# Kernel optimization log

Measured on AMD Instinct MI355X. Metric: run time of the kernel, lower is better.

The kernel has to match this reference:

```python
import math
import jax, jax.numpy as jnp
import numpy as np

HEAD_NUM = 8
DIM = 512
D_K = DIM // HEAD_NUM  # 64
M_FEAT = 256
B, L = 4, 2048
STAB = 1e-5


def _orthogonal_gaussian(m, d, rng):
    num_squares = m // d
    blocks = []
    for _ in range(num_squares):
        q, _ = np.linalg.qr(rng.standard_normal((d, d)))
        blocks.append(q.T)
    rem = m - d * num_squares
    if rem:
        q, _ = np.linalg.qr(rng.standard_normal((d, d)))
        blocks.append(q.T[:rem])
    mat = np.concatenate(blocks, axis=0)
    mat = mat / math.sqrt(num_squares + rem / d)
    return mat.astype(np.float32)


def setup_inputs() -> dict:
    key = jax.random.key(0)
    ks = jax.random.split(key, 12)
    rng = np.random.default_rng(0)
    inp = {
        'query': jax.random.normal(ks[0], (B, L, DIM), jnp.float32),
        'key': jax.random.normal(ks[1], (B, L, DIM), jnp.float32),
        'value': jax.random.normal(ks[2], (B, L, DIM), jnp.float32),
        'proj': jnp.asarray(_orthogonal_gaussian(M_FEAT, D_K, rng)),  # [M, d_k]
        'w_q_w': jax.random.normal(ks[3], (DIM, DIM), jnp.float32) * 0.02,
        'w_q_b': jnp.zeros((DIM,), jnp.float32),
        'w_k_w': jax.random.normal(ks[4], (DIM, DIM), jnp.float32) * 0.02,
        'w_k_b': jnp.zeros((DIM,), jnp.float32),
        'w_v_w': jax.random.normal(ks[5], (DIM, DIM), jnp.float32) * 0.02,
        'w_v_b': jnp.zeros((DIM,), jnp.float32),
        'w_o_w': jax.random.normal(ks[6], (DIM, DIM), jnp.float32) * 0.02,
        'w_o_b': jnp.zeros((DIM,), jnp.float32),
    }
    return inp


def _relu_kernel(data, proj):
    # data: [B,L,H,D], proj: [M,D] -> [B,L,H,M]
    ratio = 1.0 / math.sqrt(proj.shape[0])
    return jax.nn.relu(ratio * jnp.einsum('blhd,md->blhm', data, proj)) + STAB


def _favor_causal(qp, kp, vs):
    # qp, kp: [L,B,H,M]; vs: [L,B,H,D] -> num [L,B,H,D], den [L,B,H]
    b, h, m = qp.shape[1], qp.shape[2], qp.shape[3]
    d = vs.shape[3]
    carry0 = (jnp.zeros((b, h, m, d), qp.dtype), jnp.zeros((b, h, m), qp.dtype))

    def step(carry, inp):
        s_kv, s_k = carry
        q_l, k_l, v_l = inp
        s_kv = s_kv + jnp.einsum('bhm,bhd->bhmd', k_l, v_l)
        s_k = s_k + k_l
        num = jnp.einsum('bhmd,bhm->bhd', s_kv, q_l)
        den = jnp.sum(q_l * s_k, axis=-1)
        return (s_kv, s_k), (num, den)

    _, (num, den) = jax.lax.scan(step, carry0, (qp, kp, vs))
    return num, den


def reference(query, key, value, proj, w_q_w, w_q_b, w_k_w, w_k_b, w_v_w, w_v_b, w_o_w, w_o_b):
    bsz = query.shape[0]
    q = (query @ w_q_w.T + w_q_b).reshape(bsz, -1, HEAD_NUM, D_K)
    k = (key @ w_k_w.T + w_k_b).reshape(bsz, -1, HEAD_NUM, D_K)
    v = (value @ w_v_w.T + w_v_b).reshape(bsz, -1, HEAD_NUM, D_K)
    qp = jnp.swapaxes(_relu_kernel(q, proj), 0, 1)  # [L,B,H,M]
    kp = jnp.swapaxes(_relu_kernel(k, proj), 0, 1)
    vs = jnp.swapaxes(v, 0, 1)                      # [L,B,H,D]
    num, den = _favor_causal(qp, kp, vs)
    attn = jnp.swapaxes(num, 0, 1) / jnp.swapaxes(den, 0, 1)[..., None]  # [B,L,H,D]
    attn = attn.reshape(bsz, -1, HEAD_NUM * D_K)
    return attn @ w_o_w.T + w_o_b
```

## Files before the change

kernel.cpp:

```cpp
#include <hip/hip_runtime.h>
#include <stdint.h>

#define B_ 4
#define L_ 2048
#define H_ 8
#define DK 64
#define M_ 256
#define DIM_ 512
#define NTOK (B_ * L_)
#define CHK 128
#define NC (L_ / CHK)
#define BH (B_ * H_)
#define RATIO 0.0625f
#define STABC 1e-5f

typedef unsigned short ushort_t;
typedef __attribute__((ext_vector_type(8))) short bf8v;
typedef __attribute__((ext_vector_type(4))) float f4v;

#define MFMA16(a, b, c) __builtin_amdgcn_mfma_f32_16x16x32_bf16(a, b, c, 0, 0, 0)

__device__ __forceinline__ ushort_t f2bf(float f) {
  uint32_t u = __float_as_uint(f);
  return (ushort_t)((u + 0x7fffu + ((u >> 16) & 1u)) >> 16);
}
__device__ __forceinline__ float bf2f(ushort_t u) { return __uint_as_float(((uint32_t)u) << 16); }

__device__ __forceinline__ void gll16(const void* g, void* l) {
  __builtin_amdgcn_global_load_lds((const __attribute__((address_space(1))) void*)g,
                                   (__attribute__((address_space(3))) void*)l, 16, 0, 0);
}

__device__ __forceinline__ bf8v ldfrag(const ushort_t* base, int row, int cb) {
  return *(const bf8v*)((const char*)base + row * 128 + (cb ^ ((row & 7) << 4)));
}
__device__ __forceinline__ bf8v ldfrag256(const ushort_t* base, int row, int cb) {
  return *(const bf8v*)((const char*)base + row * 256 + (cb ^ ((row & 7) << 4)));
}
__device__ __forceinline__ bf8v ldfrag512(const ushort_t* base, int row, int cb) {
  return *(const bf8v*)((const char*)base + row * 512 + (cb ^ ((row & 7) << 4)));
}

__global__ __launch_bounds__(256) void cvt_w(const float* __restrict__ wq, const float* __restrict__ wk,
                                             const float* __restrict__ wv, const float* __restrict__ wo,
                                             const float* __restrict__ pj, ushort_t* __restrict__ d) {
  int i = (blockIdx.x * 256 + threadIdx.x) * 8;
  const float* s;
  int off;
  if (i < 262144)       { s = wq; off = i; }
  else if (i < 524288)  { s = wk; off = i - 262144; }
  else if (i < 786432)  { s = wv; off = i - 524288; }
  else if (i < 1048576) { s = wo; off = i - 786432; }
  else                  { s = pj; off = i - 1048576; }
  float4 a = *(const float4*)(s + off);
  float4 b = *(const float4*)(s + off + 4);
  union { ushort_t u[8]; uint4 vv; } o;
  o.u[0] = f2bf(a.x); o.u[1] = f2bf(a.y); o.u[2] = f2bf(a.z); o.u[3] = f2bf(a.w);
  o.u[4] = f2bf(b.x); o.u[5] = f2bf(b.y); o.u[6] = f2bf(b.z); o.u[7] = f2bf(b.w);
  *(uint4*)(d + i) = o.vv;
}

__global__ __launch_bounds__(256) void qkvgemm_k(const float* __restrict__ q, const float* __restrict__ k,
                                                 const float* __restrict__ v, const ushort_t* __restrict__ Wc,
                                                 const float* __restrict__ bq, const float* __restrict__ bk,
                                                 const float* __restrict__ bv, ushort_t* __restrict__ XHq,
                                                 ushort_t* __restrict__ XHk, ushort_t* __restrict__ VT) {
  __shared__ char SB[65536];
  ushort_t* Tt = (ushort_t*)SB;
  const int flat = blockIdx.x + (blockIdx.y << 6) + (blockIdx.z << 8);
  const int xcd = flat & 7, sl = flat >> 3;
  const int p = sl >> 2, bnn = sl & 3;
  const int idx = xcd * 24 + p;
  const int z = idx >> 6;
  const int bm = (idx & 63) * 128, bn = bnn * 128;
  const float* X = (z == 0) ? q : (z == 1) ? k : v;
  const ushort_t* Bw = Wc + (size_t)z * 262144;
  const float* bias = (z == 0) ? bq : (z == 1) ? bk : bv;
  const int tid = threadIdx.x, lane = tid & 63, w = tid >> 6;
  const int srow = w * 8 + (lane >> 3);
  const int scol = (((lane & 7) * 16) ^ ((lane >> 3) << 4)) >> 1;
  const int wr = (w >> 1) * 64, wc = (w & 1) * 64;
  const int fr = lane & 15, ks = lane >> 4, fq = lane >> 4;
  f4v acc[4][4] = {};
  {
#pragma unroll
    for (int i = 0; i < 4; ++i)
      gll16(Bw + (size_t)(bn + i * 32 + srow) * DIM_ + scol, SB + 32768 + i * 4096 + w * 1024);
#pragma unroll
    for (int i = 0; i < 4; ++i) {
      int e = tid + i * 256;
      int r = e >> 3, g = e & 7;
      const float* src = X + (size_t)(bm + r) * DIM_ + g * 8;
      float4 f0 = *(const float4*)src;
      float4 f1 = *(const float4*)(src + 4);
      union { ushort_t u[8]; bf8v v8; } pk;
      pk.u[0] = f2bf(f0.x); pk.u[1] = f2bf(f0.y); pk.u[2] = f2bf(f0.z); pk.u[3] = f2bf(f0.w);
      pk.u[4] = f2bf(f1.x); pk.u[5] = f2bf(f1.y); pk.u[6] = f2bf(f1.z); pk.u[7] = f2bf(f1.w);
      *(bf8v*)(SB + r * 128 + ((g * 16) ^ ((r & 7) << 4))) = pk.v8;
    }
  }
  __syncthreads();
  for (int t = 0; t < 8; ++t) {
    const ushort_t* curA = (const ushort_t*)(SB + (t & 1) * 16384);
    const ushort_t* curB = (const ushort_t*)(SB + 32768 + (t & 1) * 16384);
    char* nxtA = SB + ((t + 1) & 1) * 16384;
    char* nxtB = SB + 32768 + ((t + 1) & 1) * 16384;
    const int nk = (t + 1) * 64;
    float4 fA[4][2];
    if (t < 7) {
#pragma unroll
      for (int i = 0; i < 4; ++i) {
        int e = tid + i * 256;
        int r = e >> 3, g = e & 7;
        const float* src = X + (size_t)(bm + r) * DIM_ + nk + g * 8;
        fA[i][0] = *(const float4*)src;
        fA[i][1] = *(const float4*)(src + 4);
      }
#pragma unroll
      for (int i = 0; i < 4; ++i)
        gll16(Bw + (size_t)(bn + i * 32 + srow) * DIM_ + nk + scol, nxtB + i * 4096 + w * 1024);
    }
#pragma unroll
    for (int kk = 0; kk < 2; ++kk) {
      const int cb = kk * 64 + ks * 16;
      bf8v av[4], bv2[4];
#pragma unroll
      for (int m = 0; m < 4; ++m) av[m] = ldfrag(curA, wr + m * 16 + fr, cb);
#pragma unroll
      for (int n = 0; n < 4; ++n) bv2[n] = ldfrag(curB, wc + n * 16 + fr, cb);
#pragma unroll
      for (int m = 0; m < 4; ++m)
#pragma unroll
        for (int n = 0; n < 4; ++n) acc[m][n] = MFMA16(av[m], bv2[n], acc[m][n]);
    }
    if (t < 7) {
#pragma unroll
      for (int i = 0; i < 4; ++i) {
        int e = tid + i * 256;
        int r = e >> 3, g = e & 7;
        union { ushort_t u[8]; bf8v v8; } pk;
        pk.u[0] = f2bf(fA[i][0].x); pk.u[1] = f2bf(fA[i][0].y);
        pk.u[2] = f2bf(fA[i][0].z); pk.u[3] = f2bf(fA[i][0].w);
        pk.u[4] = f2bf(fA[i][1].x); pk.u[5] = f2bf(fA[i][1].y);
        pk.u[6] = f2bf(fA[i][1].z); pk.u[7] = f2bf(fA[i][1].w);
        *(bf8v*)(nxtA + r * 128 + ((g * 16) ^ ((r & 7) << 4))) = pk.v8;
      }
    }
    __syncthreads();
  }
  if (z == 2) {
#pragma unroll
    for (int m = 0; m < 4; ++m)
#pragma unroll
      for (int n = 0; n < 4; ++n) {
        int cl = wc + n * 16 + fr;
        float bsv = bias[bn + cl];
#pragma unroll
        for (int j = 0; j < 4; ++j) {
          int rl = wr + m * 16 + fq * 4 + j;
          Tt[cl * 136 + rl] = f2bf(acc[m][n][j] + bsv);
        }
      }
    __syncthreads();
    const int dl = tid >> 1, seg = tid & 1;
    const int c = bn + dl;
    const int bh2 = (bm >> 11) * 8 + (c >> 6);
    const int drow = c & 63;
    size_t vbase = ((size_t)(bh2 * 64 + drow)) * L_ + (bm & 2047) + seg * 64;
#pragma unroll
    for (int qq = 0; qq < 8; ++qq)
      *(uint4*)&VT[vbase + qq * 8] = *(const uint4*)&Tt[dl * 136 + seg * 64 + qq * 8];
  } else {
    ushort_t* Y = (z == 0) ? XHq : XHk;
#pragma unroll
    for (int m = 0; m < 4; ++m)
#pragma unroll
      for (int n = 0; n < 4; ++n) {
        int col = bn + wc + n * 16 + fr;
        float bsv = bias[col];
#pragma unroll
        for (int j = 0; j < 4; ++j) {
          int row = bm + wr + m * 16 + fq * 4 + j;
          Y[(size_t)row * DIM_ + col] = f2bf(acc[m][n][j] + bsv);
        }
      }
  }
}

__global__ __launch_bounds__(256) void cp2_k(const ushort_t* __restrict__ XHk, const ushort_t* __restrict__ P,
                                             const ushort_t* __restrict__ VT, ushort_t* __restrict__ S) {
  __shared__ ushort_t Ps[256 * 64];
  __shared__ ushort_t Xs[128 * 64];
  __shared__ ushort_t Kt[256 * 128];
  const int ci = blockIdx.x, bh = blockIdx.y;
  const int b = bh >> 3, h = bh & 7;
  const int tid = threadIdx.x, lane = tid & 63, w = tid >> 6;
  const int srow = w * 8 + (lane >> 3);
  const int scol = (((lane & 7) * 16) ^ ((lane >> 3) << 4)) >> 1;
  const int fr = lane & 15, ks = lane >> 4, fq = lane >> 4;
  const int l0 = ci * CHK;
#pragma unroll
  for (int i = 0; i < 8; ++i)
    gll16(P + (size_t)(i * 32 + srow) * 64 + scol, (char*)Ps + i * 4096 + w * 1024);
#pragma unroll
  for (int i = 0; i < 4; ++i)
    gll16(XHk + (size_t)(b * L_ + l0 + i * 32 + srow) * DIM_ + h * 64 + scol, (char*)Xs + i * 4096 + w * 1024);
  __syncthreads();
  {
    f4v acc[4][8] = {};
#pragma unroll
    for (int kk = 0; kk < 2; ++kk) {
      const int cb = kk * 64 + ks * 16;
      bf8v av[4], bv[8];
#pragma unroll
      for (int m = 0; m < 4; ++m) av[m] = ldfrag(Ps, w * 64 + m * 16 + fr, cb);
#pragma unroll
      for (int n = 0; n < 8; ++n) bv[n] = ldfrag(Xs, n * 16 + fr, cb);
#pragma unroll
      for (int m = 0; m < 4; ++m)
#pragma unroll
        for (int n = 0; n < 8; ++n) acc[m][n] = MFMA16(av[m], bv[n], acc[m][n]);
    }
#pragma unroll
    for (int m = 0; m < 4; ++m)
#pragma unroll
      for (int n = 0; n < 8; ++n) {
        const int mb = w * 64 + m * 16 + fq * 4;
        const int ll = n * 16 + fr;
#pragma unroll
        for (int j = 0; j < 4; ++j) {
          float v = fmaxf(RATIO * acc[m][n][j], 0.f) + STABC;
          *(ushort_t*)((char*)Kt + (mb + j) * 256 + ((ll * 2) ^ (((mb + j) & 7) << 4))) = f2bf(v);
        }
      }
  }
  __syncthreads();
  f4v accS[5][4] = {};
  for (int kt = 0; kt < 2; ++kt) {
#pragma unroll
    for (int i = 0; i < 2; ++i)
      gll16(VT + ((size_t)bh * 64 + i * 32 + srow) * L_ + l0 + kt * 64 + scol, (char*)Xs + i * 4096 + w * 1024);
    if (tid < 32) ((uint32_t*)Xs)[2048 + tid] = 0x3f803f80u;
    __syncthreads();
#pragma unroll
    for (int kk = 0; kk < 2; ++kk) {
      const int cbA = kk * 64 + ks * 16;
      const int cbK = kt * 128 + kk * 64 + ks * 16;
      bf8v av[5], bv[4];
#pragma unroll
      for (int a = 0; a < 5; ++a) av[a] = ldfrag(Xs, a * 16 + fr, cbA);
#pragma unroll
      for (int n = 0; n < 4; ++n) bv[n] = ldfrag256(Kt, w * 64 + n * 16 + fr, cbK);
#pragma unroll
      for (int a = 0; a < 5; ++a)
#pragma unroll
        for (int n = 0; n < 4; ++n) accS[a][n] = MFMA16(av[a], bv[n], accS[a][n]);
    }
    __syncthreads();
  }
  const size_t base = ((size_t)bh * NC + ci) * 65;
#pragma unroll
  for (int a = 0; a < 5; ++a)
#pragma unroll
    for (int n = 0; n < 4; ++n)
#pragma unroll
      for (int j = 0; j < 4; ++j) {
        int row = a * 16 + fq * 4 + j;
        if (row < 65) S[(base + row) * M_ + w * 64 + n * 16 + fr] = f2bf(accS[a][n][j]);
      }
}

__global__ __launch_bounds__(256) void prefix2_k(ushort_t* __restrict__ S) {
  const int g = blockIdx.x * 256 + threadIdx.x;
  const int bh = g / 2080, r = g - bh * 2080;
  ushort_t* base = S + (size_t)bh * (NC * 65 * M_) + (size_t)r * 8;
  uint4 v[16];
#pragma unroll
  for (int ci = 0; ci < NC; ++ci) v[ci] = *(const uint4*)(base + (size_t)ci * (65 * M_));
  float c[8] = {};
#pragma unroll
  for (int ci = 0; ci < NC; ++ci) {
    union { uint4 u; ushort_t s[8]; } in, out;
    in.u = v[ci];
#pragma unroll
    for (int e = 0; e < 8; ++e) {
      float t = bf2f(in.s[e]);
      out.s[e] = f2bf(c[e]);
      c[e] += t;
    }
    *(uint4*)(base + (size_t)ci * (65 * M_)) = out.u;
  }
}

__global__ __launch_bounds__(512) void qkout4_k(const ushort_t* __restrict__ XHq, const ushort_t* __restrict__ XHk,
                                                const ushort_t* __restrict__ P, const ushort_t* __restrict__ VT,
                                                const ushort_t* __restrict__ S, ushort_t* __restrict__ attn) {
  __shared__ char LB[147456];
  ushort_t* Qp  = (ushort_t*)LB;
  ushort_t* Pj  = (ushort_t*)(LB + 65536);
  ushort_t* Kps = (ushort_t*)(LB + 98304);
  ushort_t* R2  = (ushort_t*)(LB + 114688);
  ushort_t* Xk  = (ushort_t*)(LB + 131072);
  const int ci = blockIdx.x, bh = blockIdx.y;
  const int b = bh >> 3, h = bh & 7;
  const int tid = threadIdx.x, lane = tid & 63, w = tid >> 6;
  const int srow = w * 8 + (lane >> 3);
  const int scol = (((lane & 7) * 16) ^ ((lane >> 3) << 4)) >> 1;
  const int fr = lane & 15, ks = lane >> 4, fq = lane >> 4;
  const int l0 = ci * CHK;
  const size_t tokb = (size_t)b * L_ + l0;
  const size_t sbase = ((size_t)bh * NC + ci) * 65;
#pragma unroll
  for (int i = 0; i < 4; ++i)
    gll16(P + (size_t)(i * 64 + srow) * 64 + scol, (char*)Pj + i * 8192 + w * 1024);
#pragma unroll
  for (int i = 0; i < 2; ++i) {
    gll16(XHq + (tokb + i * 64 + srow) * DIM_ + h * 64 + scol, (char*)R2 + i * 8192 + w * 1024);
    gll16(XHk + (tokb + i * 64 + srow) * DIM_ + h * 64 + scol, (char*)Xk + i * 8192 + w * 1024);
  }
  __syncthreads();
  {
    f4v accF[2][8] = {};
#pragma unroll
    for (int kk = 0; kk < 2; ++kk) {
      const int cb = kk * 64 + ks * 16;
      bf8v av[2], bv[8];
#pragma unroll
      for (int m = 0; m < 2; ++m) av[m] = ldfrag(Pj, w * 32 + m * 16 + fr, cb);
#pragma unroll
      for (int n = 0; n < 8; ++n) bv[n] = ldfrag(R2, n * 16 + fr, cb);
#pragma unroll
      for (int m = 0; m < 2; ++m)
#pragma unroll
        for (int n = 0; n < 8; ++n) accF[m][n] = MFMA16(av[m], bv[n], accF[m][n]);
    }
#pragma unroll
    for (int m = 0; m < 2; ++m)
#pragma unroll
      for (int n = 0; n < 8; ++n) {
        const int mb = w * 32 + m * 16 + fq * 4;
        const int ll = n * 16 + fr;
        ushort_t bvv[4];
#pragma unroll
        for (int j = 0; j < 4; ++j)
          bvv[j] = f2bf(fmaxf(RATIO * accF[m][n][j], 0.f) + STABC);
        uint2 pk;
        pk.x = (uint32_t)bvv[0] | ((uint32_t)bvv[1] << 16);
        pk.y = (uint32_t)bvv[2] | ((uint32_t)bvv[3] << 16);
        *(uint2*)((char*)Qp + ll * 512 + ((mb * 2) ^ ((ll & 7) << 4))) = pk;
      }
  }
  __syncthreads();
  const int qr = (w & 3) * 32, qc = (w >> 2) * 64;
  const int orow = w * 16;
  f4v accA[2][4] = {};
  f4v acc2[5] = {};
  for (int kt = 0; kt < 4; ++kt) {
    gll16(S + (sbase + srow) * M_ + kt * 64 + scol, (char*)R2 + w * 1024);
    if (tid < 32)
      ((uint32_t*)R2)[2048 + tid] = ((const uint32_t*)(S + (sbase + 64) * M_ + kt * 64))[tid];
    {
      const int fi = w >> 1, tf0 = (w & 1) * 4;
      f4v accK[4] = {};
#pragma unroll
      for (int kk = 0; kk < 2; ++kk) {
        const int cb = kk * 64 + ks * 16;
        bf8v ap = ldfrag(Pj, kt * 64 + fi * 16 + fr, cb);
        bf8v bx[4];
#pragma unroll
        for (int t2 = 0; t2 < 4; ++t2) bx[t2] = ldfrag(Xk, (tf0 + t2) * 16 + fr, cb);
#pragma unroll
        for (int t2 = 0; t2 < 4; ++t2) accK[t2] = MFMA16(ap, bx[t2], accK[t2]);
      }
#pragma unroll
      for (int t2 = 0; t2 < 4; ++t2) {
        const int tt = (tf0 + t2) * 16 + fr;
        const int fl = fi * 16 + fq * 4;
#pragma unroll
        for (int j = 0; j < 4; ++j) {
          float v = fmaxf(RATIO * accK[t2][j], 0.f) + STABC;
          *(ushort_t*)((char*)Kps + tt * 128 + (((fl + j) * 2) ^ ((tt & 7) << 4))) = f2bf(v);
        }
      }
    }
    __syncthreads();
#pragma unroll
    for (int kk = 0; kk < 2; ++kk) {
      const int cb = kk * 64 + ks * 16;
      const int cbQ = kt * 128 + cb;
      bf8v aq[2], bk_[4], a2, sv[5];
#pragma unroll
      for (int m = 0; m < 2; ++m) aq[m] = ldfrag512(Qp, qr + m * 16 + fr, cbQ);
#pragma unroll
      for (int n = 0; n < 4; ++n) bk_[n] = ldfrag(Kps, qc + n * 16 + fr, cb);
#pragma unroll
      for (int m = 0; m < 2; ++m)
#pragma unroll
        for (int n = 0; n < 4; ++n) accA[m][n] = MFMA16(aq[m], bk_[n], accA[m][n]);
      a2 = ldfrag512(Qp, orow + fr, cbQ);
#pragma unroll
      for (int n = 0; n < 5; ++n) sv[n] = ldfrag(R2, n * 16 + fr, cb);
#pragma unroll
      for (int n = 0; n < 5; ++n) acc2[n] = MFMA16(a2, sv[n], acc2[n]);
    }
    __syncthreads();
  }
#pragma unroll
  for (int m = 0; m < 2; ++m)
#pragma unroll
    for (int n = 0; n < 4; ++n)
#pragma unroll
      for (int j = 0; j < 4; ++j) {
        int row = qr + m * 16 + fq * 4 + j;
        int col = qc + n * 16 + fr;
        float v = (col <= row) ? accA[m][n][j] : 0.f;
        *(ushort_t*)((char*)Pj + row * 256 + ((col * 2) ^ ((row & 7) << 4))) = f2bf(v);
      }
  __syncthreads();
  for (int kt2 = 0; kt2 < 2; ++kt2) {
    gll16(VT + ((size_t)bh * 64 + srow) * L_ + l0 + kt2 * 64 + scol, (char*)R2 + w * 1024);
    if (tid < 32) ((uint32_t*)R2)[2048 + tid] = 0x3f803f80u;
    __syncthreads();
#pragma unroll
    for (int kk = 0; kk < 2; ++kk) {
      const int cb = kk * 64 + ks * 16;
      bf8v a3, sv[5];
      a3 = ldfrag256(Pj, orow + fr, kt2 * 128 + cb);
#pragma unroll
      for (int n = 0; n < 5; ++n) sv[n] = ldfrag(R2, n * 16 + fr, cb);
#pragma unroll
      for (int n = 0; n < 5; ++n) acc2[n] = MFMA16(a3, sv[n], acc2[n]);
    }
    __syncthreads();
  }
  float dinv[4];
#pragma unroll
  for (int j = 0; j < 4; ++j) {
    float den = __shfl(acc2[4][j], (lane & 48));
    dinv[j] = 1.f / den;
  }
#pragma unroll
  for (int n = 0; n < 4; ++n)
#pragma unroll
    for (int j = 0; j < 4; ++j) {
      int l = orow + fq * 4 + j;
      int col = h * 64 + n * 16 + fr;
      attn[(tokb + l) * DIM_ + col] = f2bf(acc2[n][j] * dinv[j]);
    }
}

__global__ __launch_bounds__(256) void gemmo_k(const ushort_t* __restrict__ A, const ushort_t* __restrict__ Bw,
                                               const float* __restrict__ bias, float* __restrict__ Y) {
  __shared__ char SB[49152];
  const int tid = threadIdx.x, lane = tid & 63, w = tid >> 6;
  const int bm = blockIdx.x * 128, bn = blockIdx.y * 64;
  const int srow = w * 8 + (lane >> 3);
  const int scol = (((lane & 7) * 16) ^ ((lane >> 3) << 4)) >> 1;
  const int wr = (w >> 1) * 64, wc = (w & 1) * 32;
  const int fr = lane & 15, ks = lane >> 4, fq = lane >> 4;
  f4v acc[4][2] = {};
#pragma unroll
  for (int i = 0; i < 4; ++i)
    gll16(A + (size_t)(bm + i * 32 + srow) * DIM_ + scol, SB + i * 4096 + w * 1024);
#pragma unroll
  for (int i = 0; i < 2; ++i)
    gll16(Bw + (size_t)(bn + i * 32 + srow) * DIM_ + scol, SB + 32768 + i * 4096 + w * 1024);
  __syncthreads();
  for (int t = 0; t < 8; ++t) {
    const ushort_t* curA = (const ushort_t*)(SB + (t & 1) * 16384);
    const ushort_t* curB = (const ushort_t*)(SB + 32768 + (t & 1) * 8192);
    char* nxtA = SB + ((t + 1) & 1) * 16384;
    char* nxtB = SB + 32768 + ((t + 1) & 1) * 8192;
    const int nk = (t + 1) * 64;
    if (t < 7) {
#pragma unroll
      for (int i = 0; i < 4; ++i)
        gll16(A + (size_t)(bm + i * 32 + srow) * DIM_ + nk + scol, nxtA + i * 4096 + w * 1024);
#pragma unroll
      for (int i = 0; i < 2; ++i)
        gll16(Bw + (size_t)(bn + i * 32 + srow) * DIM_ + nk + scol, nxtB + i * 4096 + w * 1024);
    }
#pragma unroll
    for (int kk = 0; kk < 2; ++kk) {
      const int cb = kk * 64 + ks * 16;
      bf8v av[4], bv[2];
#pragma unroll
      for (int m = 0; m < 4; ++m) av[m] = ldfrag(curA, wr + m * 16 + fr, cb);
#pragma unroll
      for (int n = 0; n < 2; ++n) bv[n] = ldfrag(curB, wc + n * 16 + fr, cb);
#pragma unroll
      for (int m = 0; m < 4; ++m)
#pragma unroll
        for (int n = 0; n < 2; ++n) acc[m][n] = MFMA16(av[m], bv[n], acc[m][n]);
    }
    __syncthreads();
  }
#pragma unroll
  for (int m = 0; m < 4; ++m)
#pragma unroll
    for (int n = 0; n < 2; ++n) {
      int col = bn + wc + n * 16 + fr;
      float bsv = bias[col];
#pragma unroll
      for (int j = 0; j < 4; ++j) {
        int row = bm + wr + m * 16 + fq * 4 + j;
        Y[(size_t)row * DIM_ + col] = acc[m][n][j] + bsv;
      }
    }
}

extern "C" void kernel_launch(void* const* d_in, const int* in_sizes, int n_in,
                              void* d_out, int out_size, void* d_ws, size_t ws_size,
                              hipStream_t stream) {
  const float* query = (const float*)d_in[0];
  const float* key   = (const float*)d_in[1];
  const float* value = (const float*)d_in[2];
  const float* proj  = (const float*)d_in[3];
  const float* wq = (const float*)d_in[4];
  const float* bq = (const float*)d_in[5];
  const float* wk = (const float*)d_in[6];
  const float* bk = (const float*)d_in[7];
  const float* wv = (const float*)d_in[8];
  const float* bv = (const float*)d_in[9];
  const float* wo = (const float*)d_in[10];
  const float* bo = (const float*)d_in[11];

  char* ws = (char*)d_ws;
  ushort_t* Wc   = (ushort_t*)(ws);
  ushort_t* XHq  = (ushort_t*)(ws + 2129920);
  ushort_t* XHk  = (ushort_t*)(ws + 10518528);
  ushort_t* VT   = (ushort_t*)(ws + 18907136);
  ushort_t* Skv  = (ushort_t*)(ws + 27295744);
  ushort_t* attb = (ushort_t*)(ws + 44335104);
  const ushort_t* Wo = Wc + 786432;
  const ushort_t* Pc = Wc + 1048576;

  dim3 blk(256);
  cvt_w<<<520, blk, 0, stream>>>(wq, wk, wv, wo, proj, Wc);
  qkvgemm_k<<<dim3(64, 4, 3), blk, 0, stream>>>(query, key, value, Wc, bq, bk, bv, XHq, XHk, VT);
  cp2_k<<<dim3(NC, BH), blk, 0, stream>>>(XHk, Pc, VT, Skv);
  prefix2_k<<<260, blk, 0, stream>>>(Skv);
  qkout4_k<<<dim3(NC, BH), dim3(512), 0, stream>>>(XHq, XHk, Pc, VT, Skv, attb);
  gemmo_k<<<dim3(64, 8), blk, 0, stream>>>(attb, Wo, bo, (float*)d_out);
}
```

Baseline: 99.23 us.

## Stage full weight panel in LDS and load A fragments directly from global

Measured after the change: 171.6 us. +73.0%, slower.

```diff
diff --git a/kernel.cpp b/kernel.cpp
--- a/kernel.cpp
+++ b/kernel.cpp
@@ -39,6 +39,9 @@
 }
 __device__ __forceinline__ bf8v ldfrag512(const ushort_t* base, int row, int cb) {
   return *(const bf8v*)((const char*)base + row * 512 + (cb ^ ((row & 7) << 4)));
+}
+__device__ __forceinline__ bf8v ldfrag1024(const char* base, int row, int kbyte) {
+  return *(const bf8v*)(base + row * 1024 + (kbyte ^ ((row & 7) << 4)));
 }
 
 __global__ __launch_bounds__(256) void cvt_w(const float* __restrict__ wq, const float* __restrict__ wk,
@@ -60,99 +63,67 @@
   *(uint4*)(d + i) = o.vv;
 }
 
-__global__ __launch_bounds__(256) void qkvgemm_k(const float* __restrict__ q, const float* __restrict__ k,
-                                                 const float* __restrict__ v, const ushort_t* __restrict__ Wc,
-                                                 const float* __restrict__ bq, const float* __restrict__ bk,
-                                                 const float* __restrict__ bv, ushort_t* __restrict__ XHq,
-                                                 ushort_t* __restrict__ XHk, ushort_t* __restrict__ VT) {
+__global__ __launch_bounds__(256, 2) void qkvgemm_k(const float* __restrict__ q, const float* __restrict__ k,
+                                                    const float* __restrict__ v, const ushort_t* __restrict__ Wc,
+                                                    const float* __restrict__ bq, const float* __restrict__ bk,
+                                                    const float* __restrict__ bv, ushort_t* __restrict__ XHq,
+                                                    ushort_t* __restrict__ XHk, ushort_t* __restrict__ VT) {
   __shared__ char SB[65536];
   ushort_t* Tt = (ushort_t*)SB;
-  const int flat = blockIdx.x + (blockIdx.y << 6) + (blockIdx.z << 8);
-  const int xcd = flat & 7, sl = flat >> 3;
-  const int p = sl >> 2, bnn = sl & 3;
-  const int idx = xcd * 24 + p;
-  const int z = idx >> 6;
-  const int bm = (idx & 63) * 128, bn = bnn * 128;
+  const int z = blockIdx.z;
   const float* X = (z == 0) ? q : (z == 1) ? k : v;
   const ushort_t* Bw = Wc + (size_t)z * 262144;
   const float* bias = (z == 0) ? bq : (z == 1) ? bk : bv;
   const int tid = threadIdx.x, lane = tid & 63, w = tid >> 6;
-  const int srow = w * 8 + (lane >> 3);
-  const int scol = (((lane & 7) * 16) ^ ((lane >> 3) << 4)) >> 1;
-  const int wr = (w >> 1) * 64, wc = (w & 1) * 64;
+  const int bm = blockIdx.x * 128, bn = blockIdx.y * 64;
   const int fr = lane & 15, ks = lane >> 4, fq = lane >> 4;
-  f4v acc[4][4] = {};
-  {
-#pragma unroll
-    for (int i = 0; i < 4; ++i)
-      gll16(Bw + (size_t)(bn + i * 32 + srow) * DIM_ + scol, SB + 32768 + i * 4096 + w * 1024);
-#pragma unroll
-    for (int i = 0; i < 4; ++i) {
-      int e = tid + i * 256;
-      int r = e >> 3, g = e & 7;
-      const float* src = X + (size_t)(bm + r) * DIM_ + g * 8;
-      float4 f0 = *(const float4*)src;
-      float4 f1 = *(const float4*)(src + 4);
-      union { ushort_t u[8]; bf8v v8; } pk;
-      pk.u[0] = f2bf(f0.x); pk.u[1] = f2bf(f0.y); pk.u[2] = f2bf(f0.z); pk.u[3] = f2bf(f0.w);
-      pk.u[4] = f2bf(f1.x); pk.u[5] = f2bf(f1.y); pk.u[6] = f2bf(f1.z); pk.u[7] = f2bf(f1.w);
-      *(bf8v*)(SB + r * 128 + ((g * 16) ^ ((r & 7) << 4))) = pk.v8;
-    }
-  }
-  __syncthreads();
+  const int wr = (w >> 1) * 64, wc = (w & 1) * 32;
+#pragma unroll
+  for (int i = 0; i < 16; ++i) {
+    const int row = i * 4 + w;
+    const int sc = ((lane * 16) ^ ((row & 7) << 4)) >> 1;
+    gll16(Bw + (size_t)(bn + row) * DIM_ + sc, SB + row * 1024);
+  }
+  __syncthreads();
+  f4v acc[4][2] = {};
+#pragma unroll 2
   for (int t = 0; t < 8; ++t) {
-    const ushort_t* curA = (const ushort_t*)(SB + (t & 1) * 16384);
-    const ushort_t* curB = (const ushort_t*)(SB + 32768 + (t & 1) * 16384);
-    char* nxtA = SB + ((t + 1) & 1) * 16384;
-    char* nxtB = SB + 32768 + ((t + 1) & 1) * 16384;
-    const int nk = (t + 1) * 64;
-    float4 fA[4][2];
-    if (t < 7) {
-#pragma unroll
-      for (int i = 0; i < 4; ++i) {
-        int e = tid + i * 256;
-        int r = e >> 3, g = e & 7;
-        const float* src = X + (size_t)(bm + r) * DIM_ + nk + g * 8;
-        fA[i][0] = *(const float4*)src;
-        fA[i][1] = *(const float4*)(src + 4);
-      }
-#pragma unroll
-      for (int i = 0; i < 4; ++i)
-        gll16(Bw + (size_t)(bn + i * 32 + srow) * DIM_ + nk + scol, nxtB + i * 4096 + w * 1024);
-    }
-#pragma unroll
-    for (int kk = 0; kk < 2; ++kk) {
-      const int cb = kk * 64 + ks * 16;
-      bf8v av[4], bv2[4];
-#pragma unroll
-      for (int m = 0; m < 4; ++m) av[m] = ldfrag(curA, wr + m * 16 + fr, cb);
-#pragma unroll
-      for (int n = 0; n < 4; ++n) bv2[n] = ldfrag(curB, wc + n * 16 + fr, cb);
+    const int k0 = t * 64;
+    bf8v afr[2][4];
+#pragma unroll
+    for (int m = 0; m < 4; ++m) {
+      const float* ab = X + (size_t)(bm + wr + m * 16 + fr) * DIM_ + k0 + ks * 8;
+#pragma unroll
+      for (int kk = 0; kk < 2; ++kk) {
+        float4 f0 = *(const float4*)(ab + kk * 32);
+        float4 f1 = *(const float4*)(ab + kk * 32 + 4);
+        uint32_t p0, p1, p2, p3;
+        asm("v_cvt_pk_bf16_f32 %0, %1, %2" : "=v"(p0) : "v"(f0.x), "v"(f0.y));
+        asm("v_cvt_pk_bf16_f32 %0, %1, %2" : "=v"(p1) : "v"(f0.z), "v"(f0.w));
+        asm("v_cvt_pk_bf16_f32 %0, %1, %2" : "=v"(p2) : "v"(f1.x), "v"(f1.y));
+        asm("v_cvt_pk_bf16_f32 %0, %1, %2" : "=v"(p3) : "v"(f1.z), "v"(f1.w));
+        union { uint32_t u[4]; bf8v v8; } pk = {{p0, p1, p2, p3}};
+        afr[kk][m] = pk.v8;
+      }
+    }
+#pragma unroll
+    for (int kk = 0; kk < 2; ++kk) {
+      const int kbyte = (k0 + kk * 32 + ks * 8) * 2;
+      bf8v bfr[2];
+#pragma unroll
+      for (int n = 0; n < 2; ++n) bfr[n] = ldfrag1024(SB, wc + n * 16 + fr, kbyte);
 #pragma unroll
       for (int m = 0; m < 4; ++m)
 #pragma unroll
-        for (int n = 0; n < 4; ++n) acc[m][n] = MFMA16(av[m], bv2[n], acc[m][n]);
-    }
-    if (t < 7) {
-#pragma unroll
-      for (int i = 0; i < 4; ++i) {
-        int e = tid + i * 256;
-        int r = e >> 3, g = e & 7;
-        union { ushort_t u[8]; bf8v v8; } pk;
-        pk.u[0] = f2bf(fA[i][0].x); pk.u[1] = f2bf(fA[i][0].y);
-        pk.u[2] = f2bf(fA[i][0].z); pk.u[3] = f2bf(fA[i][0].w);
-        pk.u[4] = f2bf(fA[i][1].x); pk.u[5] = f2bf(fA[i][1].y);
-        pk.u[6] = f2bf(fA[i][1].z); pk.u[7] = f2bf(fA[i][1].w);
-        *(bf8v*)(nxtA + r * 128 + ((g * 16) ^ ((r & 7) << 4))) = pk.v8;
-      }
-    }
-    __syncthreads();
+        for (int n = 0; n < 2; ++n) acc[m][n] = MFMA16(afr[kk][m], bfr[n], acc[m][n]);
+    }
   }
   if (z == 2) {
+    __syncthreads();
 #pragma unroll
     for (int m = 0; m < 4; ++m)
 #pragma unroll
-      for (int n = 0; n < 4; ++n) {
+      for (int n = 0; n < 2; ++n) {
         int cl = wc + n * 16 + fr;
         float bsv = bias[bn + cl];
 #pragma unroll
@@ -162,20 +133,18 @@
         }
       }
     __syncthreads();
-    const int dl = tid >> 1, seg = tid & 1;
-    const int c = bn + dl;
-    const int bh2 = (bm >> 11) * 8 + (c >> 6);
-    const int drow = c & 63;
-    size_t vbase = ((size_t)(bh2 * 64 + drow)) * L_ + (bm & 2047) + seg * 64;
-#pragma unroll
-    for (int qq = 0; qq < 8; ++qq)
-      *(uint4*)&VT[vbase + qq * 8] = *(const uint4*)&Tt[dl * 136 + seg * 64 + qq * 8];
+    const int d = tid >> 2, seg = tid & 3;
+    const int b = bm >> 11, h = blockIdx.y, l0 = bm & 2047;
+    size_t vbase = ((size_t)((b * 8 + h) * 64 + d)) * L_ + l0 + seg * 32;
+#pragma unroll
+    for (int qq = 0; qq < 4; ++qq)
+      *(uint4*)&VT[vbase + qq * 8] = *(const uint4*)&Tt[d * 136 + seg * 32 + qq * 8];
   } else {
     ushort_t* Y = (z == 0) ? XHq : XHk;
 #pragma unroll
     for (int m = 0; m < 4; ++m)
 #pragma unroll
-      for (int n = 0; n < 4; ++n) {
+      for (int n = 0; n < 2; ++n) {
         int col = bn + wc + n * 16 + fr;
         float bsv = bias[col];
 #pragma unroll
@@ -449,51 +418,42 @@
     }
 }
 
-__global__ __launch_bounds__(256) void gemmo_k(const ushort_t* __restrict__ A, const ushort_t* __restrict__ Bw,
-                                               const float* __restrict__ bias, float* __restrict__ Y) {
-  __shared__ char SB[49152];
+__global__ __launch_bounds__(256, 2) void gemmo_k(const ushort_t* __restrict__ A, const ushort_t* __restrict__ Bw,
+                                                  const float* __restrict__ bias, float* __restrict__ Y) {
+  __shared__ char SB[65536];
   const int tid = threadIdx.x, lane = tid & 63, w = tid >> 6;
   const int bm = blockIdx.x * 128, bn = blockIdx.y * 64;
-  const int srow = w * 8 + (lane >> 3);
-  const int scol = (((lane & 7) * 16) ^ ((lane >> 3) << 4)) >> 1;
+  const int fr = lane & 15, ks = lane >> 4, fq = lane >> 4;
   const int wr = (w >> 1) * 64, wc = (w & 1) * 32;
-  const int fr = lane & 15, ks = lane >> 4, fq = lane >> 4;
+#pragma unroll
+  for (int i = 0; i < 16; ++i) {
+    const int row = i * 4 + w;
+    const int sc = ((lane * 16) ^ ((row & 7) << 4)) >> 1;
+    gll16(Bw + (size_t)(bn + row) * DIM_ + sc, SB + row * 1024);
+  }
+  __syncthreads();
   f4v acc[4][2] = {};
-#pragma unroll
-  for (int i = 0; i < 4; ++i)
-    gll16(A + (size_t)(bm + i * 32 + srow) * DIM_ + scol, SB + i * 4096 + w * 1024);
-#pragma unroll
-  for (int i = 0; i < 2; ++i)
-    gll16(Bw + (size_t)(bn + i * 32 + srow) * DIM_ + scol, SB + 32768 + i * 4096 + w * 1024);
-  __syncthreads();
+#pragma unroll 2
   for (int t = 0; t < 8; ++t) {
-    const ushort_t* curA = (const ushort_t*)(SB + (t & 1) * 16384);
-    const ushort_t* curB = (const ushort_t*)(SB + 32768 + (t & 1) * 8192);
-    char* nxtA = SB + ((t + 1) & 1) * 16384;
-    char* nxtB = SB + 32768 + ((t + 1) & 1) * 8192;
-    const int nk = (t + 1) * 64;
-    if (t < 7) {
-#pragma unroll
-      for (int i = 0; i < 4; ++i)
-        gll16(A + (size_t)(bm + i * 32 + srow) * DIM_ + nk + scol, nxtA + i * 4096 + w * 1024);
-#pragma unroll
-      for (int i = 0; i < 2; ++i)
-        gll16(Bw + (size_t)(bn + i * 32 + srow) * DIM_ + nk + scol, nxtB + i * 4096 + w * 1024);
-    }
-#pragma unroll
-    for (int kk = 0; kk < 2; ++kk) {
-      const int cb = kk * 64 + ks * 16;
-      bf8v av[4], bv[2];
-#pragma unroll
-      for (int m = 0; m < 4; ++m) av[m] = ldfrag(curA, wr + m * 16 + fr, cb);
-#pragma unroll
-      for (int n = 0; n < 2; ++n) bv[n] = ldfrag(curB, wc + n * 16 + fr, cb);
+    const int k0 = t * 64;
+    bf8v afr[2][4];
+#pragma unroll
+    for (int m = 0; m < 4; ++m) {
+      const ushort_t* ab = A + (size_t)(bm + wr + m * 16 + fr) * DIM_ + k0 + ks * 8;
+#pragma unroll
+      for (int kk = 0; kk < 2; ++kk) afr[kk][m] = *(const bf8v*)(ab + kk * 32);
+    }
+#pragma unroll
+    for (int kk = 0; kk < 2; ++kk) {
+      const int kbyte = (k0 + kk * 32 + ks * 8) * 2;
+      bf8v bfr[2];
+#pragma unroll
+      for (int n = 0; n < 2; ++n) bfr[n] = ldfrag1024(SB, wc + n * 16 + fr, kbyte);
 #pragma unroll
       for (int m = 0; m < 4; ++m)
 #pragma unroll
-        for (int n = 0; n < 2; ++n) acc[m][n] = MFMA16(av[m], bv[n], acc[m][n]);
-    }
-    __syncthreads();
+        for (int n = 0; n < 2; ++n) acc[m][n] = MFMA16(afr[kk][m], bfr[n], acc[m][n]);
+    }
   }
 #pragma unroll
   for (int m = 0; m < 4; ++m)
@@ -537,7 +497,7 @@
 
   dim3 blk(256);
   cvt_w<<<520, blk, 0, stream>>>(wq, wk, wv, wo, proj, Wc);
-  qkvgemm_k<<<dim3(64, 4, 3), blk, 0, stream>>>(query, key, value, Wc, bq, bk, bv, XHq, XHk, VT);
+  qkvgemm_k<<<dim3(64, 8, 3), blk, 0, stream>>>(query, key, value, Wc, bq, bk, bv, XHq, XHk, VT);
   cp2_k<<<dim3(NC, BH), blk, 0, stream>>>(XHk, Pc, VT, Skv);
   prefix2_k<<<260, blk, 0, stream>>>(Skv);
   qkout4_k<<<dim3(NC, BH), dim3(512), 0, stream>>>(XHq, XHk, Pc, VT, Skv, attb);
```
